# Kernel optimization log

Hardware: AMD Instinct MI355X
Metric: run time of the kernel (lower is better)

Reference implementation:

```python
import jax, jax.numpy as jnp
import numpy as np

DIM = 1024
N_HEADS = 16
HEAD_DIM = DIM // N_HEADS
SCALE = HEAD_DIM ** -0.5


def setup_inputs() -> dict:
    key = jax.random.key(0)
    ks = jax.random.split(key, 5)
    B, N = 2, 2048
    x = jax.random.normal(ks[0], (B, N, DIM), dtype=jnp.float32)
    # torch Linear: y = x @ W.T + b, W shape (out, in)
    qkv_w = jax.random.normal(ks[1], (3 * DIM, DIM), dtype=jnp.float32) * (DIM ** -0.5)
    qkv_b = jax.random.normal(ks[2], (3 * DIM,), dtype=jnp.float32) * 0.02
    proj_w = jax.random.normal(ks[3], (DIM, DIM), dtype=jnp.float32) * (DIM ** -0.5)
    proj_b = jax.random.normal(ks[4], (DIM,), dtype=jnp.float32) * 0.02
    return {"x": x, "qkv_w": qkv_w, "qkv_b": qkv_b, "proj_w": proj_w, "proj_b": proj_b}


def reference(x, qkv_w, qkv_b, proj_w, proj_b):
    B, N, D = x.shape
    qkv = x @ qkv_w.T + qkv_b                      # [B, N, 3D]
    qkv = qkv.reshape(B, N, 3, N_HEADS, HEAD_DIM)
    qkv = jnp.transpose(qkv, (2, 0, 3, 1, 4))      # [3, B, H, N, hd]
    q, k, v = qkv[0], qkv[1], qkv[2]
    dp = jnp.einsum('bhqd,bhkd->bhqk', q, k) * SCALE  # [B, H, N, N]
    attn = jax.nn.softmax(dp, axis=-1)
    wa = jnp.einsum('bhqk,bhkd->bhqd', attn, v)    # [B, H, N, hd]
    wa = jnp.transpose(wa, (0, 2, 1, 3)).reshape(B, N, D)
    return wa @ proj_w.T + proj_b
```

## Files before the change

kernel.cpp:

```cpp
#include <hip/hip_runtime.h>

#define BATCH 2
#define SEQ   2048
#define DIM   1024
#define NHEAD 16
#define HD    64
#define BH    (BATCH * NHEAD)
#define SCALE 0.125f
#define LOG2E 1.44269504f
#define NT128 (SEQ / 128)

typedef __attribute__((ext_vector_type(8))) short short8;
typedef __attribute__((ext_vector_type(4))) float f32x4;
typedef __attribute__((ext_vector_type(16))) float f32x16;
typedef __attribute__((ext_vector_type(2))) unsigned int uint2v;

#define MFMA16(a, b, c) __builtin_amdgcn_mfma_f32_16x16x32_bf16(a, b, c, 0, 0, 0)
#define MFMA32(a, b, c) __builtin_amdgcn_mfma_f32_32x32x16_bf16(a, b, c, 0, 0, 0)

__device__ __forceinline__ ushort f2bf(float f) {
    union { float f; unsigned u; } v;
    v.f = f;
    unsigned r = (v.u + 0x7FFF + ((v.u >> 16) & 1)) >> 16;
    return (ushort)r;
}

__device__ __forceinline__ uint4 ld8f_bf16(const float* p) {
    float4 f0 = *(const float4*)p;
    float4 f1 = *(const float4*)(p + 4);
    union { ushort us[8]; uint4 v; } u;
    u.us[0] = f2bf(f0.x); u.us[1] = f2bf(f0.y);
    u.us[2] = f2bf(f0.z); u.us[3] = f2bf(f0.w);
    u.us[4] = f2bf(f1.x); u.us[5] = f2bf(f1.y);
    u.us[6] = f2bf(f1.z); u.us[7] = f2bf(f1.w);
    return u.v;
}

__device__ __forceinline__ void gl_lds16(const ushort* g, ushort* l) {
    __builtin_amdgcn_global_load_lds(
        (const __attribute__((address_space(1))) unsigned int*)g,
        (__attribute__((address_space(3))) unsigned int*)l,
        16, 0, 0);
}

#define N_X  (BATCH * SEQ * DIM)
#define N_QW (3 * DIM * DIM)
#define N_PW (DIM * DIM)

__global__ __launch_bounds__(256) void cvt_kernel(
    const float* __restrict__ x, const float* __restrict__ qw,
    const float* __restrict__ pw, ushort* __restrict__ xb,
    ushort* __restrict__ qwb, ushort* __restrict__ pwb)
{
    const int i = (blockIdx.x * 256 + threadIdx.x) * 8;
    if (i < N_X)  *(uint4*)(xb  + i) = ld8f_bf16(x  + i);
    if (i < N_QW) *(uint4*)(qwb + i) = ld8f_bf16(qw + i);
    if (i < N_PW) *(uint4*)(pwb + i) = ld8f_bf16(pw + i);
}

template <int MODE, int WM, typename TOUT>
__global__ __launch_bounds__(256, 2) void gemm_bt(
    const ushort* __restrict__ A, const ushort* __restrict__ W,
    const float* __restrict__ bias, TOUT* __restrict__ out,
    int M, int Nout, int K)
{
    constexpr int BM = 2 * WM * 16;
    __shared__ __align__(16) ushort As[2][BM * 32];
    __shared__ __align__(16) ushort Bs[2][128 * 32];

    const int tid  = threadIdx.x;
    const int wave = tid >> 6, lane = tid & 63;
    const int quad = lane >> 4, l16 = lane & 15;
    const int wm = wave >> 1, wn = wave & 1;
    const int m0 = blockIdx.y * BM, n0 = blockIdx.x * 128;

    const int c0 = tid, c1 = tid + 256;
    const ushort* gA0 = A + (size_t)(m0 + (c0 >> 2)) * K + (c0 & 3) * 8;
    const ushort* gA1 = A + (size_t)(m0 + (c1 >> 2)) * K + (c1 & 3) * 8;
    const ushort* gB0 = W + (size_t)(n0 + (c0 >> 2)) * K + (c0 & 3) * 8;
    const ushort* gB1 = W + (size_t)(n0 + (c1 >> 2)) * K + (c1 & 3) * 8;

#define STAGE_G(buf, k0)                                                  \
    {                                                                     \
        gl_lds16(gA0 + (k0), &As[buf][(wave * 64) * 8]);                  \
        if (WM == 4) gl_lds16(gA1 + (k0), &As[buf][(wave * 64 + 256) * 8]); \
        gl_lds16(gB0 + (k0), &Bs[buf][(wave * 64) * 8]);                  \
        gl_lds16(gB1 + (k0), &Bs[buf][(wave * 64 + 256) * 8]);            \
    }

    f32x4 acc[WM][4];
#pragma unroll
    for (int i = 0; i < WM; i++)
#pragma unroll
        for (int j = 0; j < 4; j++) acc[i][j] = (f32x4){0.f, 0.f, 0.f, 0.f};

    const int KT = K >> 5;
    STAGE_G(0, 0)

    for (int kt = 0; kt < KT; kt++) {
        const int cur = kt & 1;
        __syncthreads();
        if (kt + 1 < KT) STAGE_G(cur ^ 1, (kt + 1) * 32)

        short8 af[WM], bfr[4];
#pragma unroll
        for (int mt = 0; mt < WM; mt++)
            af[mt] = *(const short8*)&As[cur][(wm * (WM * 16) + mt * 16 + l16) * 32 + quad * 8];
#pragma unroll
        for (int nt = 0; nt < 4; nt++)
            bfr[nt] = *(const short8*)&Bs[cur][(wn * 64 + nt * 16 + l16) * 32 + quad * 8];
#pragma unroll
        for (int mt = 0; mt < WM; mt++)
#pragma unroll
            for (int nt = 0; nt < 4; nt++)
                acc[mt][nt] = MFMA16(af[mt], bfr[nt], acc[mt][nt]);
    }

#pragma unroll
    for (int nt = 0; nt < 4; nt++) {
        const int n = n0 + wn * 64 + nt * 16 + l16;
        const float bv = bias[n];
#pragma unroll
        for (int mt = 0; mt < WM; mt++) {
            const int mBase = m0 + wm * (WM * 16) + mt * 16 + quad * 4;
#pragma unroll
            for (int r = 0; r < 4; r++) {
                const int m = mBase + r;
                float v = acc[mt][nt][r] + bv;
                if (MODE == 0) {
                    const int which = n >> 10, rem = n & 1023;
                    const int h = rem >> 6, d = rem & 63;
                    const int b = m >> 11, nq = m & 2047;
                    const int bh = b * NHEAD + h;
                    if (which == 0) v *= (SCALE * LOG2E);
                    size_t idx;
                    if (which == 2)
                        idx = (size_t)2 * BH * SEQ * HD + ((size_t)bh * HD + d) * SEQ + nq;
                    else
                        idx = (size_t)which * BH * SEQ * HD + ((size_t)bh * SEQ + nq) * HD + d;
                    ((ushort*)out)[idx] = f2bf(v);
                } else {
                    ((float*)out)[(size_t)m * Nout + n] = v;
                }
            }
        }
    }
#undef STAGE_G
}

__global__ __launch_bounds__(256, 2) void attn_kernel(
    const ushort* __restrict__ qkv, ushort* __restrict__ wa)
{
    __shared__ __align__(16) ushort Ks[2][2][64 * 64];
    __shared__ __align__(16) ushort Vs[2][2][64 * 64];

    const int tid  = threadIdx.x;
    const int wave = tid >> 6, lane = tid & 63;
    const int l31  = lane & 31, hb = lane >> 5;

    const int l = blockIdx.x;
    const int bh = (l & 7) + 8 * (l >> 7);
    const int qi = (l >> 3) & 15;
    const int b = bh >> 4, head = bh & 15;

    const size_t hOff = (size_t)bh * SEQ * HD;
    const ushort* Q  = qkv + hOff;
    const ushort* Kg = qkv + (size_t)BH * SEQ * HD + hOff;
    const ushort* Vt = qkv + (size_t)2 * BH * SEQ * HD + hOff;
    const int q0 = qi * 128 + wave * 32;

    short8 qf[4];
#pragma unroll
    for (int i = 0; i < 4; i++)
        qf[i] = *(const short8*)&Q[(size_t)(q0 + l31) * HD + i * 16 + hb * 8];

    f32x16 o0, o1;
#pragma unroll
    for (int r = 0; r < 16; r++) { o0[r] = 0.f; o1[r] = 0.f; }
    float lsum = 0.f;

    const int rr = lane >> 3;
    const int cc = ((lane & 7) ^ rr) * 8;
    const ushort* KgL = Kg + rr * HD + cc;
    const ushort* VtL = Vt + (size_t)rr * SEQ + cc;

#define STAGE(buf, kt)                                                          \
    {                                                                           \
        const size_t kO = (size_t)(kt) * 128;                                   \
        gl_lds16(KgL + (kO +      wave * 16    ) * HD, &Ks[buf][0][(wave*16    ) * 64]); \
        gl_lds16(KgL + (kO +      wave * 16 + 8) * HD, &Ks[buf][0][(wave*16 + 8) * 64]); \
        gl_lds16(KgL + (kO + 64 + wave * 16    ) * HD, &Ks[buf][1][(wave*16    ) * 64]); \
        gl_lds16(KgL + (kO + 64 + wave * 16 + 8) * HD, &Ks[buf][1][(wave*16 + 8) * 64]); \
        gl_lds16(VtL + (size_t)(wave*16    ) * SEQ + kO,      &Vs[buf][0][(wave*16    ) * 64]); \
        gl_lds16(VtL + (size_t)(wave*16 + 8) * SEQ + kO,      &Vs[buf][0][(wave*16 + 8) * 64]); \
        gl_lds16(VtL + (size_t)(wave*16    ) * SEQ + kO + 64, &Vs[buf][1][(wave*16    ) * 64]); \
        gl_lds16(VtL + (size_t)(wave*16 + 8) * SEQ + kO + 64, &Vs[buf][1][(wave*16 + 8) * 64]); \
    }

    STAGE(0, 0)

    const int swz = l31 & 7;

    for (int kt = 0; kt < NT128; kt++) {
        const int cur = kt & 1;
        __syncthreads();
        if (kt + 1 < NT128) STAGE(cur ^ 1, kt + 1)

#pragma unroll
        for (int hh = 0; hh < 2; hh++) {
            const ushort* kb_ = &Ks[cur][hh][0];
            const ushort* vb_ = &Vs[cur][hh][0];

            f32x16 z[2];
#pragma unroll
            for (int kb = 0; kb < 2; kb++)
#pragma unroll
                for (int r = 0; r < 16; r++) z[kb][r] = 0.f;

            __builtin_amdgcn_s_setprio(1);
#pragma unroll
            for (int i = 0; i < 4; i++) {
                short8 ka0 = *(const short8*)&kb_[(l31     ) * 64 + (((2*i + hb) ^ swz) * 8)];
                short8 ka1 = *(const short8*)&kb_[(32 + l31) * 64 + (((2*i + hb) ^ swz) * 8)];
                z[0] = MFMA32(ka0, qf[i], z[0]);
                z[1] = MFMA32(ka1, qf[i], z[1]);
            }
            __builtin_amdgcn_s_setprio(0);

            unsigned u[2][8];
#pragma unroll
            for (int kb = 0; kb < 2; kb++) {
#pragma unroll
                for (int r = 0; r < 16; r++) {
                    const float pv = __builtin_amdgcn_exp2f(z[kb][r]);
                    z[kb][r] = pv;
                    lsum += pv;
                }
#pragma unroll
                for (int m = 0; m < 8; m++) {
                    unsigned pk;
                    asm("v_cvt_pk_bf16_f32 %0, %1, %2"
                        : "=v"(pk) : "v"(z[kb][2*m]), "v"(z[kb][2*m + 1]));
                    u[kb][m] = pk;
                }
            }

            __builtin_amdgcn_s_setprio(1);
#pragma unroll
            for (int i = 0; i < 4; i++) {
                const int kb = i >> 1, ii = i & 1;
                uint2v s0 = __builtin_amdgcn_permlane32_swap(
                    u[kb][4*ii + 0], u[kb][4*ii + 2], false, false);
                uint2v s1 = __builtin_amdgcn_permlane32_swap(
                    u[kb][4*ii + 1], u[kb][4*ii + 3], false, false);
                union { unsigned w[4]; short8 s; } pf;
                pf.w[0] = s0[0]; pf.w[1] = s1[0]; pf.w[2] = s0[1]; pf.w[3] = s1[1];
                short8 vb0 = *(const short8*)&vb_[(l31     ) * 64 + (((2*i + hb) ^ swz) * 8)];
                short8 vb1 = *(const short8*)&vb_[(32 + l31) * 64 + (((2*i + hb) ^ swz) * 8)];
                o0 = MFMA32(pf.s, vb0, o0);
                o1 = MFMA32(pf.s, vb1, o1);
            }
            __builtin_amdgcn_s_setprio(0);
        }
    }

    lsum += __shfl_xor(lsum, 32);
    const float invf = 1.f / lsum;

#pragma unroll
    for (int r = 0; r < 16; r++) {
        const int qr = (r & 3) + 8 * (r >> 2) + 4 * hb;
        const float iv = __shfl(invf, qr);
        ushort* dst = wa + ((size_t)(b * SEQ + q0 + qr)) * DIM + head * HD + l31;
        dst[0]  = f2bf(o0[r] * iv);
        dst[32] = f2bf(o1[r] * iv);
    }
#undef STAGE
}

extern "C" void kernel_launch(void* const* d_in, const int* in_sizes, int n_in,
                              void* d_out, int out_size, void* d_ws, size_t ws_size,
                              hipStream_t stream)
{
    const float* x      = (const float*)d_in[0];
    const float* qkv_w  = (const float*)d_in[1];
    const float* qkv_b  = (const float*)d_in[2];
    const float* proj_w = (const float*)d_in[3];
    const float* proj_b = (const float*)d_in[4];
    float* out = (float*)d_out;

    ushort* xb  = (ushort*)d_ws;
    ushort* qwb = xb  + (size_t)N_X;
    ushort* pwb = qwb + (size_t)N_QW;
    ushort* qkv = pwb + (size_t)N_PW;
    ushort* wa  = qkv + (size_t)3 * BH * SEQ * HD;

    const int M = BATCH * SEQ;
    dim3 blk(256);

    cvt_kernel<<<dim3((N_X / 8 + 255) / 256), blk, 0, stream>>>(
        x, qkv_w, proj_w, xb, qwb, pwb);

    gemm_bt<0, 4, ushort><<<dim3((3 * DIM) / 128, M / 128), blk, 0, stream>>>(
        xb, qwb, qkv_b, qkv, M, 3 * DIM, DIM);

    attn_kernel<<<dim3(512), dim3(256), 0, stream>>>(qkv, wa);

    gemm_bt<1, 2, float><<<dim3(DIM / 128, M / 64), blk, 0, stream>>>(
        wa, pwb, proj_b, out, M, DIM, DIM);
}
```

Before: 186.1 us.

## Split attention key range across two wave groups and merge partial outputs in LDS

Doubles the attention block to 512 threads. Two groups of four waves each process half of the key sequence for the same 128 queries, using separate double-buffered LDS tiles of 64 keys. At the end, the second group writes its partial O and row sums to LDS, and the first group adds them, normalizes and stores the result. This is meant to raise wave-level parallelism and latency hiding per CU, since 512 blocks give too few waves. The cost is an extra LDS reduction, extra barriers and more register pressure under the tighter launch bounds.

```diff
diff --git a/kernel.cpp b/kernel.cpp
--- a/kernel.cpp
+++ b/kernel.cpp
@@ -8,7 +8,7 @@
 #define BH    (BATCH * NHEAD)
 #define SCALE 0.125f
 #define LOG2E 1.44269504f
-#define NT128 (SEQ / 128)
+#define NTK   16
 
 typedef __attribute__((ext_vector_type(8))) short short8;
 typedef __attribute__((ext_vector_type(4))) float f32x4;
@@ -148,7 +148,7 @@
 #undef STAGE_G
 }
 
-__global__ __launch_bounds__(256, 2) void attn_kernel(
+__global__ __launch_bounds__(512, 4) void attn_kernel(
     const ushort* __restrict__ qkv, ushort* __restrict__ wa)
 {
     __shared__ __align__(16) ushort Ks[2][2][64 * 64];
@@ -157,6 +157,7 @@
     const int tid  = threadIdx.x;
     const int wave = tid >> 6, lane = tid & 63;
     const int l31  = lane & 31, hb = lane >> 5;
+    const int h2 = wave >> 2, w4 = wave & 3;
 
     const int l = blockIdx.x;
     const int bh = (l & 7) + 8 * (l >> 7);
@@ -167,7 +168,7 @@
     const ushort* Q  = qkv + hOff;
     const ushort* Kg = qkv + (size_t)BH * SEQ * HD + hOff;
     const ushort* Vt = qkv + (size_t)2 * BH * SEQ * HD + hOff;
-    const int q0 = qi * 128 + wave * 32;
+    const int q0 = qi * 128 + w4 * 32;
 
     short8 qf[4];
 #pragma unroll
@@ -177,7 +178,7 @@
     f32x16 o0, o1;
 #pragma unroll
     for (int r = 0; r < 16; r++) { o0[r] = 0.f; o1[r] = 0.f; }
-    float lsum = 0.f;
+    f32x4 lacc = (f32x4){0.f, 0.f, 0.f, 0.f};
 
     const int rr = lane >> 3;
     const int cc = ((lane & 7) ^ rr) * 8;
@@ -186,94 +187,107 @@
 
 #define STAGE(buf, kt)                                                          \
     {                                                                           \
-        const size_t kO = (size_t)(kt) * 128;                                   \
-        gl_lds16(KgL + (kO +      wave * 16    ) * HD, &Ks[buf][0][(wave*16    ) * 64]); \
-        gl_lds16(KgL + (kO +      wave * 16 + 8) * HD, &Ks[buf][0][(wave*16 + 8) * 64]); \
-        gl_lds16(KgL + (kO + 64 + wave * 16    ) * HD, &Ks[buf][1][(wave*16    ) * 64]); \
-        gl_lds16(KgL + (kO + 64 + wave * 16 + 8) * HD, &Ks[buf][1][(wave*16 + 8) * 64]); \
-        gl_lds16(VtL + (size_t)(wave*16    ) * SEQ + kO,      &Vs[buf][0][(wave*16    ) * 64]); \
-        gl_lds16(VtL + (size_t)(wave*16 + 8) * SEQ + kO,      &Vs[buf][0][(wave*16 + 8) * 64]); \
-        gl_lds16(VtL + (size_t)(wave*16    ) * SEQ + kO + 64, &Vs[buf][1][(wave*16    ) * 64]); \
-        gl_lds16(VtL + (size_t)(wave*16 + 8) * SEQ + kO + 64, &Vs[buf][1][(wave*16 + 8) * 64]); \
+        const size_t kO = (size_t)h2 * 1024 + (size_t)(kt) * 64;                \
+        gl_lds16(KgL + (kO + w4 * 16    ) * HD, &Ks[h2][buf][(w4 * 16    ) * 64]); \
+        gl_lds16(KgL + (kO + w4 * 16 + 8) * HD, &Ks[h2][buf][(w4 * 16 + 8) * 64]); \
+        gl_lds16(VtL + (size_t)(w4 * 16    ) * SEQ + kO, &Vs[h2][buf][(w4 * 16    ) * 64]); \
+        gl_lds16(VtL + (size_t)(w4 * 16 + 8) * SEQ + kO, &Vs[h2][buf][(w4 * 16 + 8) * 64]); \
     }
 
     STAGE(0, 0)
 
     const int swz = l31 & 7;
 
-    for (int kt = 0; kt < NT128; kt++) {
+    for (int kt = 0; kt < NTK; kt++) {
         const int cur = kt & 1;
         __syncthreads();
-        if (kt + 1 < NT128) STAGE(cur ^ 1, kt + 1)
-
-#pragma unroll
-        for (int hh = 0; hh < 2; hh++) {
-            const ushort* kb_ = &Ks[cur][hh][0];
-            const ushort* vb_ = &Vs[cur][hh][0];
-
-            f32x16 z[2];
-#pragma unroll
-            for (int kb = 0; kb < 2; kb++)
-#pragma unroll
-                for (int r = 0; r < 16; r++) z[kb][r] = 0.f;
-
-            __builtin_amdgcn_s_setprio(1);
-#pragma unroll
-            for (int i = 0; i < 4; i++) {
-                short8 ka0 = *(const short8*)&kb_[(l31     ) * 64 + (((2*i + hb) ^ swz) * 8)];
-                short8 ka1 = *(const short8*)&kb_[(32 + l31) * 64 + (((2*i + hb) ^ swz) * 8)];
-                z[0] = MFMA32(ka0, qf[i], z[0]);
-                z[1] = MFMA32(ka1, qf[i], z[1]);
-            }
-            __builtin_amdgcn_s_setprio(0);
-
-            unsigned u[2][8];
-#pragma unroll
-            for (int kb = 0; kb < 2; kb++) {
-#pragma unroll
-                for (int r = 0; r < 16; r++) {
-                    const float pv = __builtin_amdgcn_exp2f(z[kb][r]);
-                    z[kb][r] = pv;
-                    lsum += pv;
-                }
-#pragma unroll
-                for (int m = 0; m < 8; m++) {
-                    unsigned pk;
-                    asm("v_cvt_pk_bf16_f32 %0, %1, %2"
-                        : "=v"(pk) : "v"(z[kb][2*m]), "v"(z[kb][2*m + 1]));
-                    u[kb][m] = pk;
-                }
-            }
-
-            __builtin_amdgcn_s_setprio(1);
-#pragma unroll
-            for (int i = 0; i < 4; i++) {
-                const int kb = i >> 1, ii = i & 1;
-                uint2v s0 = __builtin_amdgcn_permlane32_swap(
-                    u[kb][4*ii + 0], u[kb][4*ii + 2], false, false);
-                uint2v s1 = __builtin_amdgcn_permlane32_swap(
-                    u[kb][4*ii + 1], u[kb][4*ii + 3], false, false);
-                union { unsigned w[4]; short8 s; } pf;
-                pf.w[0] = s0[0]; pf.w[1] = s1[0]; pf.w[2] = s0[1]; pf.w[3] = s1[1];
-                short8 vb0 = *(const short8*)&vb_[(l31     ) * 64 + (((2*i + hb) ^ swz) * 8)];
-                short8 vb1 = *(const short8*)&vb_[(32 + l31) * 64 + (((2*i + hb) ^ swz) * 8)];
-                o0 = MFMA32(pf.s, vb0, o0);
-                o1 = MFMA32(pf.s, vb1, o1);
-            }
-            __builtin_amdgcn_s_setprio(0);
-        }
-    }
-
+        if (kt + 1 < NTK) STAGE(cur ^ 1, kt + 1)
+
+        const ushort* kb_ = &Ks[h2][cur][0];
+        const ushort* vb_ = &Vs[h2][cur][0];
+
+        f32x16 z0, z1;
+#pragma unroll
+        for (int r = 0; r < 16; r++) { z0[r] = 0.f; z1[r] = 0.f; }
+
+        __builtin_amdgcn_s_setprio(1);
+#pragma unroll
+        for (int i = 0; i < 4; i++) {
+            short8 ka0 = *(const short8*)&kb_[(l31     ) * 64 + (((2*i + hb) ^ swz) * 8)];
+            short8 ka1 = *(const short8*)&kb_[(32 + l31) * 64 + (((2*i + hb) ^ swz) * 8)];
+            z0 = MFMA32(ka0, qf[i], z0);
+            z1 = MFMA32(ka1, qf[i], z1);
+        }
+        __builtin_amdgcn_s_setprio(0);
+
+        unsigned u[2][8];
+#pragma unroll
+        for (int r = 0; r < 16; r++) {
+            const float p0 = __builtin_amdgcn_exp2f(z0[r]);
+            const float p1 = __builtin_amdgcn_exp2f(z1[r]);
+            z0[r] = p0; z1[r] = p1;
+            lacc[r & 3] += p0 + p1;
+        }
+#pragma unroll
+        for (int m = 0; m < 8; m++) {
+            unsigned pk;
+            asm("v_cvt_pk_bf16_f32 %0, %1, %2"
+                : "=v"(pk) : "v"(z0[2*m]), "v"(z0[2*m + 1]));
+            u[0][m] = pk;
+            asm("v_cvt_pk_bf16_f32 %0, %1, %2"
+                : "=v"(pk) : "v"(z1[2*m]), "v"(z1[2*m + 1]));
+            u[1][m] = pk;
+        }
+
+        __builtin_amdgcn_s_setprio(1);
+#pragma unroll
+        for (int i = 0; i < 4; i++) {
+            const int kb = i >> 1, ii = i & 1;
+            uint2v s0 = __builtin_amdgcn_permlane32_swap(
+                u[kb][4*ii + 0], u[kb][4*ii + 2], false, false);
+            uint2v s1 = __builtin_amdgcn_permlane32_swap(
+                u[kb][4*ii + 1], u[kb][4*ii + 3], false, false);
+            union { unsigned w[4]; short8 s; } pf;
+            pf.w[0] = s0[0]; pf.w[1] = s1[0]; pf.w[2] = s0[1]; pf.w[3] = s1[1];
+            short8 vb0 = *(const short8*)&vb_[(l31     ) * 64 + (((2*i + hb) ^ swz) * 8)];
+            short8 vb1 = *(const short8*)&vb_[(32 + l31) * 64 + (((2*i + hb) ^ swz) * 8)];
+            o0 = MFMA32(pf.s, vb0, o0);
+            o1 = MFMA32(pf.s, vb1, o1);
+        }
+        __builtin_amdgcn_s_setprio(0);
+    }
+
+    __syncthreads();
+
+    float* Osc = (float*)&Ks[0][0][0];
+    float* Lsc = (float*)&Vs[0][0][0];
+
+    float lsum = lacc[0] + lacc[1] + lacc[2] + lacc[3];
     lsum += __shfl_xor(lsum, 32);
-    const float invf = 1.f / lsum;
-
-#pragma unroll
-    for (int r = 0; r < 16; r++) {
-        const int qr = (r & 3) + 8 * (r >> 2) + 4 * hb;
-        const float iv = __shfl(invf, qr);
-        ushort* dst = wa + ((size_t)(b * SEQ + q0 + qr)) * DIM + head * HD + l31;
-        dst[0]  = f2bf(o0[r] * iv);
-        dst[32] = f2bf(o1[r] * iv);
+    if (lane < 32) Lsc[wave * 32 + l31] = lsum;
+
+    if (h2 == 1) {
+#pragma unroll
+        for (int r = 0; r < 16; r++) {
+            const int qr = (r & 3) + 8 * (r >> 2) + 4 * hb;
+            Osc[w4 * 2048 + qr * 64 + l31]      = o0[r];
+            Osc[w4 * 2048 + qr * 64 + 32 + l31] = o1[r];
+        }
+    }
+    __syncthreads();
+
+    if (h2 == 0) {
+        const float inv = 1.f / (Lsc[w4 * 32 + l31] + Lsc[(4 + w4) * 32 + l31]);
+#pragma unroll
+        for (int r = 0; r < 16; r++) {
+            const int qr = (r & 3) + 8 * (r >> 2) + 4 * hb;
+            const float iv = __shfl(inv, qr);
+            const float v0 = o0[r] + Osc[w4 * 2048 + qr * 64 + l31];
+            const float v1 = o1[r] + Osc[w4 * 2048 + qr * 64 + 32 + l31];
+            ushort* dst = wa + ((size_t)(b * SEQ + q0 + qr)) * DIM + head * HD + l31;
+            dst[0]  = f2bf(v0 * iv);
+            dst[32] = f2bf(v1 * iv);
+        }
     }
 #undef STAGE
 }
@@ -304,7 +318,7 @@
     gemm_bt<0, 4, ushort><<<dim3((3 * DIM) / 128, M / 128), blk, 0, stream>>>(
         xb, qwb, qkv_b, qkv, M, 3 * DIM, DIM);
 
-    attn_kernel<<<dim3(512), dim3(256), 0, stream>>>(qkv, wa);
+    attn_kernel<<<dim3(512), dim3(512), 0, stream>>>(qkv, wa);
 
     gemm_bt<1, 2, float><<<dim3(DIM / 128, M / 64), blk, 0, stream>>>(
         wa, pwb, proj_b, out, M, DIM, DIM);
```

New measurement: 186.7 us. About the same (+0.4%).
